# Performance work log

Hardware: AMD Instinct MI355X
Metric: run time of the kernel (lower is better)

## Reference

```python
import jax, jax.numpy as jnp
import numpy as np

B, L, E = 2, 1024, 1024
H, D = 16, 64          # num_heads, head_dim; E == H*D
KS, PAD = 3, 1         # depthwise conv kernel / padding
PROB = 0.9             # bernoulli keep-prob for key mask
NEG = -1e20


def _group(x):
    # [b, l, (h d)] -> [b, h, l, d]
    b, l, _ = x.shape
    return x.reshape(b, l, H, D).transpose(0, 2, 1, 3)


def setup_inputs() -> dict:
    key = jax.random.key(0)
    ks = jax.random.split(key, 8)
    query = jax.random.normal(ks[0], (B, L, E), jnp.float32)
    keys = jax.random.normal(ks[1], (B, L, E), jnp.float32)
    values = jax.random.normal(ks[2], (B, L, E), jnp.float32)
    padding_mask = jnp.ones((B, L, L), dtype=bool)
    causal_mask = jnp.broadcast_to(jnp.tril(jnp.ones((L, L), dtype=bool)), (B, L, L))
    ber_mask = jax.random.bernoulli(ks[3], PROB, (B, L))
    conv_w = jax.random.normal(ks[4], (H, 1, KS, KS), jnp.float32) * 0.2
    conv_b = jnp.zeros((H,), jnp.float32)
    bn_gamma = jnp.ones((H,), jnp.float32)
    bn_beta = jnp.zeros((H,), jnp.float32)
    w_v = jax.random.normal(ks[5], (D, D), jnp.float32) / np.sqrt(D)
    ln_gamma = jnp.ones((D,), jnp.float32)
    ln_beta = jnp.zeros((D,), jnp.float32)
    w_o = jax.random.normal(ks[6], (D, D), jnp.float32) / np.sqrt(D)
    b_o = jnp.zeros((D,), jnp.float32)
    return dict(query=query, keys=keys, values=values, padding_mask=padding_mask,
                causal_mask=causal_mask, ber_mask=ber_mask, conv_w=conv_w,
                conv_b=conv_b, bn_gamma=bn_gamma, bn_beta=bn_beta, w_v=w_v,
                ln_gamma=ln_gamma, ln_beta=ln_beta, w_o=w_o, b_o=b_o)


def reference(query, keys, values, padding_mask, causal_mask, ber_mask,
              conv_w, conv_b, bn_gamma, bn_beta, w_v, ln_gamma, ln_beta, w_o, b_o):
    gelu = lambda x: jax.nn.gelu(x, approximate=False)  # torch nn.GELU default (erf)

    # ---- query path: depthwise conv + residual, BatchNorm2d (batch stats), GELU
    qg = _group(query)  # [b, h, l, d]
    qc = jax.lax.conv_general_dilated(
        qg, conv_w, window_strides=(1, 1), padding=[(PAD, PAD), (PAD, PAD)],
        feature_group_count=H, dimension_numbers=('NCHW', 'OIHW', 'NCHW'))
    qc = qc + conv_b[None, :, None, None] + qg
    mean = qc.mean(axis=(0, 2, 3), keepdims=True)
    var = qc.var(axis=(0, 2, 3), keepdims=True)  # biased, as torch BN training
    q = gelu((qc - mean) * jax.lax.rsqrt(var + 1e-5)
             * bn_gamma[None, :, None, None] + bn_beta[None, :, None, None])

    # ---- key path: bernoulli-masked softmax over sequence, then GELU
    km = jnp.where(ber_mask[:, :, None], keys, NEG)
    k = gelu(_group(jax.nn.softmax(km, axis=-2)))  # softmax over length

    # ---- value path: per-head linear (no bias)
    v = jnp.einsum('bhld,ed->bhle', _group(values), w_v)

    # ---- GELU attention with combined padding & causal mask
    energy = gelu(jnp.einsum('bhqd,bhkd->bhqk', q, k))
    mask = padding_mask & causal_mask  # [b, q, k]
    energy = jnp.where(mask[:, None, :, :], energy, NEG)
    attn = jax.nn.softmax(energy / np.sqrt(E), axis=-1)

    # ---- attend, LayerNorm over head_dim, (dropout=identity in eval), linear
    o = jnp.einsum('bhqk,bhkd->bhqd', attn, v)
    mu = o.mean(-1, keepdims=True)
    s2 = o.var(-1, keepdims=True)
    on = (o - mu) * jax.lax.rsqrt(s2 + 1e-5) * ln_gamma + ln_beta
    out = jnp.einsum('bhqd,ed->bhqe', on, w_o) + b_o
    # [b, h, l, d] -> [b, l, (h d)]
    return out.transpose(0, 2, 1, 3).reshape(B, L, E)
```

## Files before the change

### kernel.cpp

```cpp
#include <hip/hip_runtime.h>
#include <hip/hip_bf16.h>
#include <math.h>

#define BB 2
#define HH 16
#define LL 1024
#define DD 64
#define EE 1024
#define NEGV -1e20f

typedef __attribute__((ext_vector_type(8))) short bf16x8;
typedef __attribute__((ext_vector_type(4))) float f32x4;

__device__ __forceinline__ float bf2f(__hip_bfloat16 x){ return __bfloat162float(x); }
__device__ __forceinline__ float gelu_erf(float x){
    return 0.5f * x * (1.0f + erff(x * 0.70710678118654752f));
}
__device__ __forceinline__ float gelu_sig(float x){
    float e = __expf(-1.702f * x);
    return x * __builtin_amdgcn_rcpf(1.0f + e);
}
__device__ __forceinline__ float ldx(const void* p, size_t i, int f32){
    return f32 ? ((const float*)p)[i] : bf2f(((const __hip_bfloat16*)p)[i]);
}
__device__ __forceinline__ short f2bs(float x){
    __hip_bfloat16 h = __float2bfloat16(x);
    return *(short*)&h;
}
__device__ __forceinline__ float bs2f(unsigned short u){
    return __uint_as_float(((unsigned)u) << 16);
}
__device__ __forceinline__ bf16x8 ld8b(const void* p, size_t i, int f32){
    bf16x8 r;
    if (f32){
        const float4* f = (const float4*)((const float*)p + i);
        float4 a = f[0], b = f[1];
        r[0]=f2bs(a.x); r[1]=f2bs(a.y); r[2]=f2bs(a.z); r[3]=f2bs(a.w);
        r[4]=f2bs(b.x); r[5]=f2bs(b.y); r[6]=f2bs(b.z); r[7]=f2bs(b.w);
    } else {
        r = *(const bf16x8*)((const __hip_bfloat16*)p + i);
    }
    return r;
}
__device__ __forceinline__ float redsum16(float x){
    x += __shfl_xor(x, 1); x += __shfl_xor(x, 2);
    x += __shfl_xor(x, 4); x += __shfl_xor(x, 8);
    return x;
}
__device__ __forceinline__ int detect_f32(const unsigned int* p){
    int inband = 0;
    #pragma unroll 1
    for (int w = 0; w < 64; ++w){
        unsigned int e0 = (p[w] >> 7) & 0xFFu;
        if (e0 >= 0x60u && e0 <= 0x8Eu) inband++;
    }
    return (inband >= 48) ? 0 : 1;
}
__device__ __forceinline__ int ber_code(const unsigned char* r){
    bool has_big = false, odd1 = false, nz_off = false;
    #pragma unroll 1
    for (int j = 0; j < 128; ++j){
        unsigned char c = r[j];
        if (c > 1) has_big = true;
        if ((j & 3) == 1 && c) odd1 = true;
        if ((j & 3) != 0 && c) nz_off = true;
    }
    if (has_big) return odd1 ? 2 : 3;
    return nz_off ? 0 : 1;
}
__device__ __forceinline__ float ber_val(const unsigned char* r, int i, int code){
    switch (code){
        case 0:  return r[i] ? 1.f : 0.f;
        case 1:  return (((const int*)r)[i] != 0) ? 1.f : 0.f;
        case 2:  return (((const unsigned short*)r)[i] != 0) ? 1.f : 0.f;
        default: return (((const float*)r)[i] != 0.f) ? 1.f : 0.f;
    }
}

__global__ __launch_bounds__(256, 2) void kA(const void* __restrict__ query,
                                             const void* __restrict__ conv_w,
                                             const void* __restrict__ conv_b,
                                             const void* __restrict__ keys,
                                             const unsigned char* __restrict__ ber_raw,
                                             float* __restrict__ statsP,
                                             float* __restrict__ Sp,
                                             float* __restrict__ berf,
                                             int* __restrict__ wsflag,
                                             __hip_bfloat16* __restrict__ qbf){
    __shared__ float tile[66][67];
    __shared__ float r1[256], r2[256];
    __shared__ float ss[4][64];
    __shared__ int sflag, sdet;
    int blk = blockIdx.x, t = threadIdx.x;
    if (blk < 512){
        if (t == 0){
            sflag = detect_f32((const unsigned int*)query);
            if (blk == 0) wsflag[0] = sflag;
        }
        int lt = blk & 15, h = (blk >> 4) & 15, b = blk >> 8;
        int bh = b * HH + h;
        int l0 = lt * 64;
        if (t < 66){ tile[t][0] = 0.f; tile[t][65] = 0.f; }
        __syncthreads();
        const int f32 = sflag;
        for (int i = t; i < 66 * 64; i += 256){
            int r = i >> 6, d = i & 63;
            int l = l0 - 1 + r;
            tile[r][d + 1] = (l >= 0 && l < LL)
                           ? ldx(query, ((size_t)b * LL + l) * EE + h * 64 + d, f32) : 0.f;
        }
        __syncthreads();
        float w9[9];
        #pragma unroll
        for (int i = 0; i < 9; ++i) w9[i] = ldx(conv_w, h * 9 + i, f32);
        float cb = ldx(conv_b, h, f32);
        int l = t & 63, db = t >> 6, d0 = db * 16;
        float s1 = 0.f, s2 = 0.f;
        unsigned short ob[16];
        #pragma unroll
        for (int jj = 0; jj < 16; ++jj){
            int d = d0 + jj;
            float acc = cb + tile[l + 1][d + 1];
            #pragma unroll
            for (int di = 0; di < 3; ++di)
                #pragma unroll
                for (int dj = 0; dj < 3; ++dj)
                    acc += w9[di * 3 + dj] * tile[l + di][d + dj];
            s1 += acc; s2 += acc * acc;
            ob[jj] = (unsigned short)f2bs(acc);
        }
        __hip_bfloat16* orow = qbf + ((size_t)bh * LL + l0 + l) * DD + d0;
        #pragma unroll
        for (int g = 0; g < 4; ++g){
            ushort4 u; u.x = ob[g*4]; u.y = ob[g*4+1]; u.z = ob[g*4+2]; u.w = ob[g*4+3];
            *(ushort4*)(orow + g * 4) = u;
        }
        r1[t] = s1; r2[t] = s2;
        __syncthreads();
        for (int s = 128; s > 0; s >>= 1){
            if (t < s){ r1[t] += r1[t + s]; r2[t] += r2[t + s]; }
            __syncthreads();
        }
        if (t == 0){
            statsP[h * 32 + b * 16 + lt] = r1[0];
            statsP[512 + h * 32 + b * 16 + lt] = r2[0];
        }
    } else {
        int blk2 = blk - 512;
        if (t == 0){ sflag = detect_f32((const unsigned int*)keys); sdet = ber_code(ber_raw); }
        __syncthreads();
        const int f32 = sflag, code = sdet;
        int ch = blk2 & 15, h = (blk2 >> 4) & 15, b = blk2 >> 8;
        int ex = t & 63, ly = t >> 6;
        int e = h * 64 + ex;
        float s = 0.f;
        #pragma unroll 4
        for (int l = ch * 64 + ly; l < ch * 64 + 64; l += 4){
            float keep = ber_val(ber_raw, b * LL + l, code);
            float x = (keep != 0.f) ? ldx(keys, ((size_t)b * LL + l) * EE + e, f32) : NEGV;
            s += __expf(x);
        }
        ss[ly][ex] = s;
        __syncthreads();
        if (ly == 0)
            Sp[(b * 16 + ch) * EE + e] = ss[0][ex] + ss[1][ex] + ss[2][ex] + ss[3][ex];
        if (h == 0 && t < 64)
            berf[b * LL + ch * 64 + t] = ber_val(ber_raw, b * LL + ch * 64 + t, code);
    }
}

__global__ __launch_bounds__(256, 2) void kC(const void* __restrict__ keys,
                                             const void* __restrict__ values,
                                             const void* __restrict__ w_v,
                                             const void* __restrict__ bn_g,
                                             const void* __restrict__ bn_b,
                                             const float* __restrict__ statsP,
                                             const float* __restrict__ Sp,
                                             const float* __restrict__ berf,
                                             const int* __restrict__ wsflag,
                                             __hip_bfloat16* __restrict__ qbf,
                                             __hip_bfloat16* __restrict__ kb,
                                             __hip_bfloat16* __restrict__ vbT){
    __shared__ float sinv_s[64];
    __shared__ float sc[2];
    int blk = blockIdx.x, t = threadIdx.x;
    const int f32 = wsflag[0];
    if (blk < 1024){
        int idx = blk * 256 + t;
        int i8 = idx * 8;
        int d0 = i8 & 63, l = (i8 >> 6) & 1023, h = (i8 >> 16) & 15, b = i8 >> 20;
        if (t < 64){
            float s1p = (t < 32) ? statsP[h * 32 + t] : 0.f;
            float s2p = (t < 32) ? statsP[512 + h * 32 + t] : 0.f;
            #pragma unroll
            for (int off = 16; off > 0; off >>= 1){
                s1p += __shfl_xor(s1p, off);
                s2p += __shfl_xor(s2p, off);
            }
            if (t == 0){
                const float N = (float)(BB * LL * DD);
                float mean = s1p / N;
                float var  = fmaxf(s2p / N - mean * mean, 0.f);
                float a = ldx(bn_g, h, f32) * rsqrtf(var + 1e-5f);
                sc[0] = a;
                sc[1] = ldx(bn_b, h, f32) - mean * a;
            }
            int e = h * 64 + t;
            float S = 0.f;
            #pragma unroll
            for (int ch = 0; ch < 16; ++ch) S += Sp[(b * 16 + ch) * EE + e];
            sinv_s[t] = 1.f / S;
        }
        __syncthreads();
        float bna = sc[0], bnc = sc[1];
        uint4 qr = *(uint4*)(qbf + i8);
        unsigned short* qs = (unsigned short*)&qr;
        uint4 qw;
        unsigned short* qws = (unsigned short*)&qw;
        #pragma unroll
        for (int j = 0; j < 8; ++j)
            qws[j] = (unsigned short)f2bs(gelu_erf(bs2f(qs[j]) * bna + bnc));
        *(uint4*)(qbf + i8) = qw;
        size_t kbase = ((size_t)b * LL + l) * EE + h * 64 + d0;
        float kv[8];
        if (f32){
            const float4* kp = (const float4*)((const float*)keys + kbase);
            float4 a = kp[0], c = kp[1];
            kv[0]=a.x; kv[1]=a.y; kv[2]=a.z; kv[3]=a.w;
            kv[4]=c.x; kv[5]=c.y; kv[6]=c.z; kv[7]=c.w;
        } else {
            uint4 kr = *(const uint4*)((const __hip_bfloat16*)keys + kbase);
            unsigned short* ks = (unsigned short*)&kr;
            #pragma unroll
            for (int j = 0; j < 8; ++j) kv[j] = bs2f(ks[j]);
        }
        float keep = berf[b * LL + l];
        uint4 kw;
        unsigned short* kws = (unsigned short*)&kw;
        #pragma unroll
        for (int j = 0; j < 8; ++j){
            float km = (keep != 0.f) ? kv[j] : NEGV;
            float p = __expf(km) * sinv_s[d0 + j];
            kws[j] = (unsigned short)f2bs(gelu_erf(p));
        }
        *(uint4*)(kb + i8) = kw;
    } else {
        int blk2 = blk - 1024;
        int lt = blk2 & 15, bh = blk2 >> 4;
        int h = bh & 15, b = bh >> 4;
        int w = t >> 6, lane = t & 63;
        int lid = lane & 15, quad = lane >> 4;
        int l = lt * 64 + w * 16 + lid;
        bf16x8 av[2];
        #pragma unroll
        for (int ck = 0; ck < 2; ++ck)
            av[ck] = ld8b(values, ((size_t)b * LL + l) * EE + h * 64 + ck * 32 + quad * 8, f32);
        f32x4 Dv[4];
        #pragma unroll
        for (int et = 0; et < 4; ++et){
            Dv[et] = (f32x4){0.f, 0.f, 0.f, 0.f};
            #pragma unroll
            for (int ck = 0; ck < 2; ++ck){
                bf16x8 bw = ld8b(w_v, (size_t)(et * 16 + lid) * 64 + ck * 32 + quad * 8, f32);
                Dv[et] = __builtin_amdgcn_mfma_f32_16x16x32_bf16(av[ck], bw, Dv[et], 0, 0, 0);
            }
        }
        #pragma unroll
        for (int et = 0; et < 4; ++et){
            ushort4 u;
            u.x = (unsigned short)f2bs(Dv[et][0]);
            u.y = (unsigned short)f2bs(Dv[et][1]);
            u.z = (unsigned short)f2bs(Dv[et][2]);
            u.w = (unsigned short)f2bs(Dv[et][3]);
            *(ushort4*)(vbT + ((size_t)bh * DD + et * 16 + lid) * LL + lt * 64 + w * 16 + quad * 4) = u;
        }
    }
}

__global__ __launch_bounds__(128, 4) void kD(const __hip_bfloat16* __restrict__ qbf,
                                             const __hip_bfloat16* __restrict__ kb,
                                             const __hip_bfloat16* __restrict__ vbT,
                                             const void* __restrict__ w_o,
                                             const void* __restrict__ b_o,
                                             const void* __restrict__ ln_g,
                                             const void* __restrict__ ln_b,
                                             const int* __restrict__ wsflag,
                                             void* __restrict__ out){
    __shared__ __align__(16) __hip_bfloat16 Pl[2][16][40];
    __shared__ __align__(16) float Ol[16][68];
    __shared__ __align__(16) __hip_bfloat16 onb[16][72];
    int blk = blockIdx.x;
    int qt = 63 - (blk >> 5);
    int bh = blk & 31;
    int h = bh & 15, b = bh >> 4;
    int t = threadIdx.x;
    int w = t >> 6, lane = t & 63;
    int lid = lane & 15, quad = lane >> 4;
    const int f32o = wsflag[0];

    int qrow = qt * 16 + lid;
    bf16x8 qf[2];
    #pragma unroll
    for (int ck = 0; ck < 2; ++ck)
        qf[ck] = *(const bf16x8*)(qbf + ((size_t)bh * LL + qrow) * DD + ck * 32 + quad * 8);

    const __hip_bfloat16* kbb = kb + (size_t)bh * LL * DD;
    const __hip_bfloat16* vbb = vbT + (size_t)bh * DD * LL;
    f32x4 O[4];
    #pragma unroll
    for (int nt = 0; nt < 4; ++nt) O[nt] = (f32x4){0.f, 0.f, 0.f, 0.f};
    const int qlane = qt * 16 + quad * 4;
    const int nkt = (qt >> 2) + 1;

    auto loadK = [&](int kw, bf16x8* dk){
        #pragma unroll
        for (int nt2 = 0; nt2 < 2; ++nt2)
            #pragma unroll
            for (int ck = 0; ck < 2; ++ck)
                dk[nt2 * 2 + ck] = *(const bf16x8*)(kbb
                    + (size_t)(kw + nt2 * 16 + lid) * DD + ck * 32 + quad * 8);
    };
    auto loadV = [&](int kw, bf16x8* dv){
        #pragma unroll
        for (int nt = 0; nt < 4; ++nt)
            dv[nt] = *(const bf16x8*)(vbb + (size_t)(nt * 16 + lid) * LL + kw + quad * 8);
    };

    bf16x8 kf[4], vf[4];
    loadK(w * 32, kf);
    loadV(w * 32, vf);

    for (int kt0 = 0; kt0 < nkt; ++kt0){
        bf16x8 kn[4], vn[4];
        const bool more = (kt0 + 1 < nkt);
        if (more){
            int kwn = (kt0 + 1) * 64 + w * 32;
            loadK(kwn, kn);
            loadV(kwn, vn);
        }
        int kw0 = kt0 * 64 + w * 32;
        f32x4 S[2];
        #pragma unroll
        for (int nt2 = 0; nt2 < 2; ++nt2){
            S[nt2] = (f32x4){0.f, 0.f, 0.f, 0.f};
            #pragma unroll
            for (int ck = 0; ck < 2; ++ck)
                S[nt2] = __builtin_amdgcn_mfma_f32_16x16x32_bf16(qf[ck], kf[nt2 * 2 + ck], S[nt2], 0, 0, 0);
        }
        #pragma unroll
        for (int nt2 = 0; nt2 < 2; ++nt2){
            int kcol = kw0 + nt2 * 16 + lid;
            #pragma unroll
            for (int r = 0; r < 4; ++r){
                float x = gelu_sig(S[nt2][r]) * 0.03125f;
                float p = __expf(x);
                p = (kcol <= qlane + r) ? p : 0.f;
                Pl[w][quad * 4 + r][nt2 * 16 + lid] = __float2bfloat16(p);
            }
        }
        bf16x8 pa = *(const bf16x8*)&Pl[w][lid][quad * 8];
        #pragma unroll
        for (int nt = 0; nt < 4; ++nt)
            O[nt] = __builtin_amdgcn_mfma_f32_16x16x32_bf16(pa, vf[nt], O[nt], 0, 0, 0);
        if (more){
            #pragma unroll
            for (int i = 0; i < 4; ++i){ kf[i] = kn[i]; vf[i] = vn[i]; }
        }
    }

    if (w == 1){
        #pragma unroll
        for (int nt = 0; nt < 4; ++nt)
            #pragma unroll
            for (int r = 0; r < 4; ++r)
                Ol[quad * 4 + r][nt * 16 + lid] = O[nt][r];
    }
    __syncthreads();
    if (w == 0){
        #pragma unroll
        for (int nt = 0; nt < 4; ++nt)
            #pragma unroll
            for (int r = 0; r < 4; ++r)
                O[nt][r] += Ol[quad * 4 + r][nt * 16 + lid];
        float lng_v[4], lnb_v[4];
        #pragma unroll
        for (int nt = 0; nt < 4; ++nt){
            lng_v[nt] = ldx(ln_g, nt * 16 + lid, f32o);
            lnb_v[nt] = ldx(ln_b, nt * 16 + lid, f32o);
        }
        #pragma unroll
        for (int r = 0; r < 4; ++r){
            float s = O[0][r] + O[1][r] + O[2][r] + O[3][r];
            s = redsum16(s);
            float mu = s * (1.f / 64.f);
            float vs = 0.f;
            #pragma unroll
            for (int nt = 0; nt < 4; ++nt){ float d2 = O[nt][r] - mu; vs += d2 * d2; }
            vs = redsum16(vs);
            float iv = rsqrtf(vs * (1.f / 64.f) + 1e-5f);
            #pragma unroll
            for (int nt = 0; nt < 4; ++nt){
                float on = (O[nt][r] - mu) * iv * lng_v[nt] + lnb_v[nt];
                onb[quad * 4 + r][nt * 16 + lid] = __float2bfloat16(on);
            }
        }
    }
    __syncthreads();
    bf16x8 oa0 = *(const bf16x8*)&onb[lid][quad * 8];
    bf16x8 oa1 = *(const bf16x8*)&onb[lid][32 + quad * 8];
    #pragma unroll
    for (int i = 0; i < 2; ++i){
        int et = w * 2 + i;
        float bo = ldx(b_o, et * 16 + lid, f32o);
        f32x4 R = (f32x4){bo, bo, bo, bo};
        bf16x8 bw0 = ld8b(w_o, (size_t)(et * 16 + lid) * 64 + quad * 8, f32o);
        bf16x8 bw1 = ld8b(w_o, (size_t)(et * 16 + lid) * 64 + 32 + quad * 8, f32o);
        R = __builtin_amdgcn_mfma_f32_16x16x32_bf16(oa0, bw0, R, 0, 0, 0);
        R = __builtin_amdgcn_mfma_f32_16x16x32_bf16(oa1, bw1, R, 0, 0, 0);
        #pragma unroll
        for (int r = 0; r < 4; ++r){
            size_t oidx = ((size_t)b * LL + qlane + r) * EE + h * 64 + et * 16 + lid;
            if (f32o) ((float*)out)[oidx] = R[r];
            else      ((__hip_bfloat16*)out)[oidx] = __float2bfloat16(R[r]);
        }
    }
}

extern "C" void kernel_launch(void* const* d_in, const int* in_sizes, int n_in,
                              void* d_out, int out_size, void* d_ws, size_t ws_size,
                              hipStream_t stream){
    int iq=-1, ik=-1, iv=-1, iber=-1, icw=-1, icb=-1, ibg=-1, ibb=-1,
        iwv=-1, ilg=-1, ilb=-1, iwo=-1, ibo=-1;
    int nbig=0, n16=0, n4096=0, n64=0;
    for (int i = 0; i < n_in; ++i){
        int s = in_sizes[i];
        if (s == BB*LL*EE){ if (nbig==0) iq=i; else if (nbig==1) ik=i; else if (nbig==2) iv=i; nbig++; }
        else if (s == BB*LL) iber = i;
        else if (s == HH*9)  icw = i;
        else if (s == HH){ if (n16==0) icb=i; else if (n16==1) ibg=i; else ibb=i; n16++; }
        else if (s == DD*DD){ if (n4096==0) iwv=i; else iwo=i; n4096++; }
        else if (s == DD){ if (n64==0) ilg=i; else if (n64==1) ilb=i; else ibo=i; n64++; }
    }
    if (iq<0||ik<0||iv<0||iber<0||icw<0||icb<0||ibg<0||ibb<0||iwv<0||ilg<0||ilb<0||iwo<0||ibo<0){
        iq=0; ik=1; iv=2; iber=5; icw=6; icb=7; ibg=8; ibb=9; iwv=10; ilg=11; ilb=12; iwo=13; ibo=14;
    }

    const size_t NEL = (size_t)BB * HH * LL * DD;
    __hip_bfloat16* qbf = (__hip_bfloat16*)d_ws;
    __hip_bfloat16* kbw = qbf + NEL;
    __hip_bfloat16* vbT = kbw + NEL;
    float* f     = (float*)(vbT + NEL);
    float* berf  = f;
    float* statsP= f + 2048;
    float* Sp    = f + 3072;
    int*   wsflag= (int*)(f + 35840);

    hipLaunchKernelGGL(kA, dim3(1024), dim3(256), 0, stream,
                       d_in[iq], d_in[icw], d_in[icb], d_in[ik],
                       (const unsigned char*)d_in[iber], statsP, Sp, berf, wsflag, qbf);
    hipLaunchKernelGGL(kC, dim3(1536), dim3(256), 0, stream,
                       d_in[ik], d_in[iv], d_in[iwv], d_in[ibg], d_in[ibb],
                       statsP, Sp, berf, wsflag, qbf, kbw, vbT);
    hipLaunchKernelGGL(kD, dim3(2048), dim3(128), 0, stream,
                       qbf, kbw, vbT, d_in[iwo], d_in[ibo], d_in[ilg], d_in[ilb],
                       wsflag, d_out);
}
```

Baseline: 183.9 us.

## Move value projection into first kernel and fuse BN+GELU into attention Q load

New measurement: 182.5 us. Within noise of the previous version (-0.7%).

```diff
diff --git a/kernel.cpp b/kernel.cpp
--- a/kernel.cpp
+++ b/kernel.cpp
@@ -81,12 +81,15 @@
                                              const void* __restrict__ conv_w,
                                              const void* __restrict__ conv_b,
                                              const void* __restrict__ keys,
+                                             const void* __restrict__ values,
+                                             const void* __restrict__ w_v,
                                              const unsigned char* __restrict__ ber_raw,
                                              float* __restrict__ statsP,
                                              float* __restrict__ Sp,
                                              float* __restrict__ berf,
                                              int* __restrict__ wsflag,
-                                             __hip_bfloat16* __restrict__ qbf){
+                                             __hip_bfloat16* __restrict__ qbf,
+                                             __hip_bfloat16* __restrict__ vbT){
     __shared__ float tile[66][67];
     __shared__ float r1[256], r2[256];
     __shared__ float ss[4][64];
@@ -145,7 +148,7 @@
             statsP[h * 32 + b * 16 + lt] = r1[0];
             statsP[512 + h * 32 + b * 16 + lt] = r2[0];
         }
-    } else {
+    } else if (blk < 1024){
         int blk2 = blk - 512;
         if (t == 0){ sflag = detect_f32((const unsigned int*)keys); sdet = ber_code(ber_raw); }
         __syncthreads();
@@ -166,85 +169,10 @@
             Sp[(b * 16 + ch) * EE + e] = ss[0][ex] + ss[1][ex] + ss[2][ex] + ss[3][ex];
         if (h == 0 && t < 64)
             berf[b * LL + ch * 64 + t] = ber_val(ber_raw, b * LL + ch * 64 + t, code);
-    }
-}
-
-__global__ __launch_bounds__(256, 2) void kC(const void* __restrict__ keys,
-                                             const void* __restrict__ values,
-                                             const void* __restrict__ w_v,
-                                             const void* __restrict__ bn_g,
-                                             const void* __restrict__ bn_b,
-                                             const float* __restrict__ statsP,
-                                             const float* __restrict__ Sp,
-                                             const float* __restrict__ berf,
-                                             const int* __restrict__ wsflag,
-                                             __hip_bfloat16* __restrict__ qbf,
-                                             __hip_bfloat16* __restrict__ kb,
-                                             __hip_bfloat16* __restrict__ vbT){
-    __shared__ float sinv_s[64];
-    __shared__ float sc[2];
-    int blk = blockIdx.x, t = threadIdx.x;
-    const int f32 = wsflag[0];
-    if (blk < 1024){
-        int idx = blk * 256 + t;
-        int i8 = idx * 8;
-        int d0 = i8 & 63, l = (i8 >> 6) & 1023, h = (i8 >> 16) & 15, b = i8 >> 20;
-        if (t < 64){
-            float s1p = (t < 32) ? statsP[h * 32 + t] : 0.f;
-            float s2p = (t < 32) ? statsP[512 + h * 32 + t] : 0.f;
-            #pragma unroll
-            for (int off = 16; off > 0; off >>= 1){
-                s1p += __shfl_xor(s1p, off);
-                s2p += __shfl_xor(s2p, off);
-            }
-            if (t == 0){
-                const float N = (float)(BB * LL * DD);
-                float mean = s1p / N;
-                float var  = fmaxf(s2p / N - mean * mean, 0.f);
-                float a = ldx(bn_g, h, f32) * rsqrtf(var + 1e-5f);
-                sc[0] = a;
-                sc[1] = ldx(bn_b, h, f32) - mean * a;
-            }
-            int e = h * 64 + t;
-            float S = 0.f;
-            #pragma unroll
-            for (int ch = 0; ch < 16; ++ch) S += Sp[(b * 16 + ch) * EE + e];
-            sinv_s[t] = 1.f / S;
-        }
-        __syncthreads();
-        float bna = sc[0], bnc = sc[1];
-        uint4 qr = *(uint4*)(qbf + i8);
-        unsigned short* qs = (unsigned short*)&qr;
-        uint4 qw;
-        unsigned short* qws = (unsigned short*)&qw;
-        #pragma unroll
-        for (int j = 0; j < 8; ++j)
-            qws[j] = (unsigned short)f2bs(gelu_erf(bs2f(qs[j]) * bna + bnc));
-        *(uint4*)(qbf + i8) = qw;
-        size_t kbase = ((size_t)b * LL + l) * EE + h * 64 + d0;
-        float kv[8];
-        if (f32){
-            const float4* kp = (const float4*)((const float*)keys + kbase);
-            float4 a = kp[0], c = kp[1];
-            kv[0]=a.x; kv[1]=a.y; kv[2]=a.z; kv[3]=a.w;
-            kv[4]=c.x; kv[5]=c.y; kv[6]=c.z; kv[7]=c.w;
-        } else {
-            uint4 kr = *(const uint4*)((const __hip_bfloat16*)keys + kbase);
-            unsigned short* ks = (unsigned short*)&kr;
-            #pragma unroll
-            for (int j = 0; j < 8; ++j) kv[j] = bs2f(ks[j]);
-        }
-        float keep = berf[b * LL + l];
-        uint4 kw;
-        unsigned short* kws = (unsigned short*)&kw;
-        #pragma unroll
-        for (int j = 0; j < 8; ++j){
-            float km = (keep != 0.f) ? kv[j] : NEGV;
-            float p = __expf(km) * sinv_s[d0 + j];
-            kws[j] = (unsigned short)f2bs(gelu_erf(p));
-        }
-        *(uint4*)(kb + i8) = kw;
     } else {
+        if (t == 0) sflag = detect_f32((const unsigned int*)values);
+        __syncthreads();
+        const int f32 = sflag;
         int blk2 = blk - 1024;
         int lt = blk2 & 15, bh = blk2 >> 4;
         int h = bh & 15, b = bh >> 4;
@@ -275,6 +203,68 @@
             *(ushort4*)(vbT + ((size_t)bh * DD + et * 16 + lid) * LL + lt * 64 + w * 16 + quad * 4) = u;
         }
     }
+}
+
+__global__ __launch_bounds__(256, 2) void kB(const void* __restrict__ keys,
+                                             const void* __restrict__ bn_g,
+                                             const void* __restrict__ bn_b,
+                                             const float* __restrict__ statsP,
+                                             const float* __restrict__ Sp,
+                                             const float* __restrict__ berf,
+                                             const int* __restrict__ wsflag,
+                                             __hip_bfloat16* __restrict__ kb,
+                                             float* __restrict__ coef){
+    __shared__ float sinv_s[64];
+    int blk = blockIdx.x, t = threadIdx.x;
+    const int f32 = wsflag[0];
+    if (blk == 0 && t < HH){
+        int h = t;
+        float s1 = 0.f, s2 = 0.f;
+        #pragma unroll 1
+        for (int j = 0; j < 32; ++j){
+            s1 += statsP[h * 32 + j];
+            s2 += statsP[512 + h * 32 + j];
+        }
+        const float N = (float)(BB * LL * DD);
+        float mean = s1 / N;
+        float var  = fmaxf(s2 / N - mean * mean, 0.f);
+        float a = ldx(bn_g, h, f32) * rsqrtf(var + 1e-5f);
+        coef[h] = a;
+        coef[16 + h] = ldx(bn_b, h, f32) - mean * a;
+    }
+    int i8 = (blk * 256 + t) * 8;
+    int d0 = i8 & 63, l = (i8 >> 6) & 1023, h = (i8 >> 16) & 15, b = i8 >> 20;
+    if (t < 64){
+        int e = h * 64 + t;
+        float S = 0.f;
+        #pragma unroll
+        for (int ch = 0; ch < 16; ++ch) S += Sp[(b * 16 + ch) * EE + e];
+        sinv_s[t] = 1.f / S;
+    }
+    __syncthreads();
+    size_t kbase = ((size_t)b * LL + l) * EE + h * 64 + d0;
+    float kv[8];
+    if (f32){
+        const float4* kp = (const float4*)((const float*)keys + kbase);
+        float4 a = kp[0], c = kp[1];
+        kv[0]=a.x; kv[1]=a.y; kv[2]=a.z; kv[3]=a.w;
+        kv[4]=c.x; kv[5]=c.y; kv[6]=c.z; kv[7]=c.w;
+    } else {
+        uint4 kr = *(const uint4*)((const __hip_bfloat16*)keys + kbase);
+        unsigned short* ks = (unsigned short*)&kr;
+        #pragma unroll
+        for (int j = 0; j < 8; ++j) kv[j] = bs2f(ks[j]);
+    }
+    float keep = berf[b * LL + l];
+    uint4 kw;
+    unsigned short* kws = (unsigned short*)&kw;
+    #pragma unroll
+    for (int j = 0; j < 8; ++j){
+        float km = (keep != 0.f) ? kv[j] : NEGV;
+        float p = __expf(km) * sinv_s[d0 + j];
+        kws[j] = (unsigned short)f2bs(gelu_erf(p));
+    }
+    *(uint4*)(kb + i8) = kw;
 }
 
 __global__ __launch_bounds__(128, 4) void kD(const __hip_bfloat16* __restrict__ qbf,
@@ -285,6 +275,7 @@
                                              const void* __restrict__ ln_g,
                                              const void* __restrict__ ln_b,
                                              const int* __restrict__ wsflag,
+                                             const float* __restrict__ coef,
                                              void* __restrict__ out){
     __shared__ __align__(16) __hip_bfloat16 Pl[2][16][40];
     __shared__ __align__(16) float Ol[16][68];
@@ -299,10 +290,15 @@
     const int f32o = wsflag[0];
 
     int qrow = qt * 16 + lid;
+    float bna = coef[h], bnc = coef[16 + h];
     bf16x8 qf[2];
     #pragma unroll
-    for (int ck = 0; ck < 2; ++ck)
-        qf[ck] = *(const bf16x8*)(qbf + ((size_t)bh * LL + qrow) * DD + ck * 32 + quad * 8);
+    for (int ck = 0; ck < 2; ++ck){
+        bf16x8 raw = *(const bf16x8*)(qbf + ((size_t)bh * LL + qrow) * DD + ck * 32 + quad * 8);
+        #pragma unroll
+        for (int j = 0; j < 8; ++j)
+            qf[ck][j] = f2bs(gelu_erf(bs2f((unsigned short)raw[j]) * bna + bnc));
+    }
 
     const __hip_bfloat16* kbb = kb + (size_t)bh * LL * DD;
     const __hip_bfloat16* vbb = vbT + (size_t)bh * DD * LL;
@@ -454,14 +450,16 @@
     float* statsP= f + 2048;
     float* Sp    = f + 3072;
     int*   wsflag= (int*)(f + 35840);
-
-    hipLaunchKernelGGL(kA, dim3(1024), dim3(256), 0, stream,
-                       d_in[iq], d_in[icw], d_in[icb], d_in[ik],
-                       (const unsigned char*)d_in[iber], statsP, Sp, berf, wsflag, qbf);
-    hipLaunchKernelGGL(kC, dim3(1536), dim3(256), 0, stream,
-                       d_in[ik], d_in[iv], d_in[iwv], d_in[ibg], d_in[ibb],
-                       statsP, Sp, berf, wsflag, qbf, kbw, vbT);
+    float* coef  = f + 35856;
+
+    hipLaunchKernelGGL(kA, dim3(1536), dim3(256), 0, stream,
+                       d_in[iq], d_in[icw], d_in[icb], d_in[ik], d_in[iv], d_in[iwv],
+                       (const unsigned char*)d_in[iber], statsP, Sp, berf, wsflag,
+                       qbf, vbT);
+    hipLaunchKernelGGL(kB, dim3(1024), dim3(256), 0, stream,
+                       d_in[ik], d_in[ibg], d_in[ibb], statsP, Sp, berf, wsflag,
+                       kbw, coef);
     hipLaunchKernelGGL(kD, dim3(2048), dim3(128), 0, stream,
                        qbf, kbw, vbT, d_in[iwo], d_in[ibo], d_in[ilg], d_in[ilb],
-                       wsflag, d_out);
-}
+                       wsflag, coef, d_out);
+}
```
